# Kernel optimization log

Hardware: AMD Instinct MI355X
Metric: run time of the kernel (lower is better)

The kernel has to match this reference:

```python
import jax, jax.numpy as jnp
import numpy as np

EPS_DEMOD = 1e-8
EPS_GN = 1e-5
GROUPS = 8


def setup_inputs() -> dict:
    key = jax.random.key(0)
    ks = jax.random.split(key, 4)
    b, c, h, w = 16, 64, 256, 256
    n_kernels, c_out = 4, 64
    x = jax.random.normal(ks[0], (b, c, h, w), dtype=jnp.float32)
    mod = jax.random.normal(ks[1], (b, c), dtype=jnp.float32)
    kernel_mod = jax.random.normal(ks[2], (b, n_kernels), dtype=jnp.float32)
    # kaiming normal, fan_in = c*3*3, leaky_relu gain sqrt(2)
    std = float(np.sqrt(2.0 / (c * 9)))
    conv_weights = jax.random.normal(ks[3], (n_kernels, c_out, c, 3, 3), dtype=jnp.float32) * std
    gn_gamma = jnp.ones((c_out,), dtype=jnp.float32)
    gn_beta = jnp.zeros((c_out,), dtype=jnp.float32)
    return {"x": x, "mod": mod, "kernel_mod": kernel_mod,
            "conv_weights": conv_weights, "gn_gamma": gn_gamma, "gn_beta": gn_beta}


def _block_forward(x, mod, kernel_mod, conv_weights, gn_gamma, gn_beta):
    b = x.shape[0]
    # --- adaptive kernel selection (softmax over num_conv_kernels) ---
    kernel_attn = jax.nn.softmax(kernel_mod, axis=-1)                # [b, n]
    w = jnp.einsum('noikl,bn->boikl', conv_weights, kernel_attn)     # [b, o, i, 3, 3]
    # --- stylegan2 modulation ---
    w = w * (mod[:, None, :, None, None] + 1.0)
    # --- demodulation ---
    inv_norm = jax.lax.rsqrt(jnp.clip(jnp.sum(w * w, axis=(2, 3, 4), keepdims=True), EPS_DEMOD, None))
    w = w * inv_norm
    # --- per-sample conv (vmap over batch, SAME padding, stride 1) ---
    def conv_one(xi, wi):
        return jax.lax.conv_general_dilated(
            xi[None], wi, window_strides=(1, 1), padding='SAME',
            dimension_numbers=('NCHW', 'OIHW', 'NCHW'))[0]
    y = jax.vmap(conv_one)(x, w)                                     # [b, o, h, w]
    # --- GroupNorm(groups=8) ---
    bb, c, hh, ww = y.shape
    yg = y.reshape(bb, GROUPS, c // GROUPS, hh, ww)
    mean = jnp.mean(yg, axis=(2, 3, 4), keepdims=True)
    var = jnp.var(yg, axis=(2, 3, 4), keepdims=True)
    yg = (yg - mean) * jax.lax.rsqrt(var + EPS_GN)
    y = yg.reshape(bb, c, hh, ww) * gn_gamma[None, :, None, None] + gn_beta[None, :, None, None]
    # --- SiLU ---
    return y * jax.nn.sigmoid(y)


def reference(x, mod, kernel_mod, conv_weights, gn_gamma, gn_beta):
    return _block_forward(x, mod, kernel_mod, conv_weights, gn_gamma, gn_beta)
```

## Files before the change

kernel.cpp:

```cpp
#include <hip/hip_runtime.h>
#include <hip/hip_bf16.h>
#include <math.h>

#define B_ 16
#define C_IN 64
#define C_OUT 64
#define H_ 256
#define W_ 256
#define NK 4
#define NGROUPS 8
#define CH_PER_G (C_OUT / NGROUPS)

#define WM16_SHORTS (B_ * C_OUT * 9 * C_IN)
#define WM16_BYTES (WM16_SHORTS * 2)
#define STATS_FLOATS (B_ * NGROUPS * 2)

#define XT_PIX (258 * 258)
#define XT_OFF ((size_t)(WM16_BYTES + 4096))
#define XT_BYTES ((size_t)B_ * XT_PIX * 64 * 2)

typedef __attribute__((ext_vector_type(8))) short bf16x8;
typedef __attribute__((ext_vector_type(4))) float f32x4;
typedef unsigned int u32;

static __device__ __forceinline__ unsigned bf16bits(float v) {
    return (unsigned)__builtin_bit_cast(unsigned short, __float2bfloat16(v));
}

static __device__ __forceinline__ void load_lds16(const unsigned short* g, void* l) {
    __builtin_amdgcn_global_load_lds(
        (const __attribute__((address_space(1))) u32*)g,
        (__attribute__((address_space(3))) u32*)l, 16, 0, 0);
}

__global__ __launch_bounds__(64)
void k_weights(const float* __restrict__ mod, const float* __restrict__ kmod,
               const float* __restrict__ cw, unsigned short* __restrict__ wm16) {
    int bo = blockIdx.x;
    int b = bo >> 6, o = bo & 63;
    int lane = threadIdx.x;

    float a0 = kmod[b * NK + 0], a1 = kmod[b * NK + 1];
    float a2 = kmod[b * NK + 2], a3 = kmod[b * NK + 3];
    float m = fmaxf(fmaxf(a0, a1), fmaxf(a2, a3));
    float e0 = __expf(a0 - m), e1 = __expf(a1 - m);
    float e2 = __expf(a2 - m), e3 = __expf(a3 - m);
    float inv = 1.0f / (e0 + e1 + e2 + e3);
    e0 *= inv; e1 *= inv; e2 *= inv; e3 *= inv;

    float modv = mod[b * C_IN + lane] + 1.0f;

    float wv[9];
    float ss = 0.0f;
#pragma unroll
    for (int j = 0; j < 9; ++j) {
        int idx = o * 576 + lane * 9 + j;
        float w = cw[0 * C_OUT * 576 + idx] * e0
                + cw[1 * C_OUT * 576 + idx] * e1
                + cw[2 * C_OUT * 576 + idx] * e2
                + cw[3 * C_OUT * 576 + idx] * e3;
        w *= modv;
        wv[j] = w;
        ss += w * w;
    }
#pragma unroll
    for (int off = 32; off > 0; off >>= 1)
        ss += __shfl_xor(ss, off, 64);
    float invn = rsqrtf(fmaxf(ss, 1e-8f));
#pragma unroll
    for (int j = 0; j < 9; ++j)
        wm16[((b * 64 + o) * 9 + j) * 64 + lane] =
            (unsigned short)bf16bits(wv[j] * invn);
}

__global__ __launch_bounds__(256)
void k_border(unsigned short* __restrict__ xt) {
    int t = blockIdx.x * 256 + threadIdx.x;
    int chunk = t & 7;
    int p = t >> 3;
    int b = p / 1028;
    int pid = p - b * 1028;
    int r, c;
    if (pid < 258)      { r = 0;             c = pid; }
    else if (pid < 516) { r = 257;           c = pid - 258; }
    else if (pid < 772) { r = pid - 516 + 1; c = 0; }
    else                { r = pid - 772 + 1; c = 257; }
    *(int4*)((char*)xt + (size_t)(b * XT_PIX + r * 258 + c) * 128 + chunk * 16) =
        make_int4(0, 0, 0, 0);
}

__global__ __launch_bounds__(256)
void k_xpose(const float* __restrict__ x, unsigned short* __restrict__ xt) {
    const int bx  = blockIdx.x;
    const int seg = bx & 1;
    const int h   = (bx >> 1) & 255;
    const int b   = bx >> 9;
    const int c   = threadIdx.x & 63;
    const int wv  = threadIdx.x >> 6;
    const int p0  = seg * 128 + wv * 32;
    const float* xp = x + (((b * 64 + c) * 256 + h) * 256 + p0);
    unsigned short* op = xt + ((size_t)(b * 258 + h + 1) * 258 + p0 + 1) * 64 + c;
#pragma unroll
    for (int j = 0; j < 8; ++j) {
        float4 v = *(const float4*)(xp + j * 4);
        op[(j * 4 + 0) * 64] = (unsigned short)bf16bits(v.x);
        op[(j * 4 + 1) * 64] = (unsigned short)bf16bits(v.y);
        op[(j * 4 + 2) * 64] = (unsigned short)bf16bits(v.z);
        op[(j * 4 + 3) * 64] = (unsigned short)bf16bits(v.w);
    }
}

#define NSLOT 340
#define SLOTPAD 352

__global__ __launch_bounds__(256, 3)
void k_conv2(const unsigned short* __restrict__ xt,
             const unsigned short* __restrict__ wm16,
             float* __restrict__ y, float* __restrict__ stats) {
    __shared__ __align__(16) char smem[SLOTPAD * 128];
    __shared__ float lst[16];

    const int tile = blockIdx.x;
    const int b    = blockIdx.y;
    const int R0   = (tile >> 3) * 8;
    const int C0   = (tile & 7) * 32;
    const int tid  = threadIdx.x;
    const int w    = tid >> 6;
    const int lane = tid & 63;
    const int l15  = lane & 15;
    const int q    = lane >> 4;

    if (tid < 16) lst[tid] = 0.0f;

    const unsigned short* xb = xt + (size_t)b * (XT_PIX * 64);
#pragma unroll
    for (int k = 0; k < 11; ++k) {
        int t = k * 256 + tid;
        int slot = t >> 3;
        int p = t & 7;
        int s = slot < NSLOT ? slot : NSLOT - 1;
        int r = s / 34;
        int c = s - r * 34;
        int srcchunk = p ^ (s & 7);
        const unsigned short* src = xb + (((R0 + r) * 258 + (C0 + c)) * 64 + srcchunk * 8);
        load_lds16(src, smem + t * 16);
    }
    __syncthreads();

    f32x4 acc[4][4];
#pragma unroll
    for (int mt = 0; mt < 4; ++mt)
#pragma unroll
        for (int nt = 0; nt < 4; ++nt)
            acc[mt][nt] = (f32x4){0.f, 0.f, 0.f, 0.f};

    const unsigned short* wb = wm16 + b * (64 * 9 * 64);

    for (int tap = 0; tap < 9; ++tap) {
        const int ky = tap / 3;
        const int kx = tap - ky * 3;

        bf16x8 af[4][2];
#pragma unroll
        for (int mt = 0; mt < 4; ++mt)
#pragma unroll
            for (int kc = 0; kc < 2; ++kc)
                af[mt][kc] = *(const bf16x8*)(wb +
                    ((mt * 16 + l15) * 9 + tap) * 64 + kc * 32 + q * 8);

#pragma unroll
        for (int kc = 0; kc < 2; ++kc) {
            bf16x8 bfr[4];
#pragma unroll
            for (int nt = 0; nt < 4; ++nt) {
                int ro = 2 * w + (nt >> 1);
                int c0 = (nt & 1) * 16;
                int slot = (ro + ky) * 34 + c0 + kx + l15;
                int chunk = kc * 4 + q;
                bfr[nt] = *(const bf16x8*)(smem + slot * 128 +
                                           ((chunk ^ (slot & 7)) << 4));
            }
#pragma unroll
            for (int mt = 0; mt < 4; ++mt)
#pragma unroll
                for (int nt = 0; nt < 4; ++nt)
                    acc[mt][nt] = __builtin_amdgcn_mfma_f32_16x16x32_bf16(
                        af[mt][kc], bfr[nt], acc[mt][nt], 0, 0, 0);
        }
    }

    float sg[4] = {0.f, 0.f, 0.f, 0.f};
    float qg[4] = {0.f, 0.f, 0.f, 0.f};
#pragma unroll
    for (int mt = 0; mt < 4; ++mt) {
#pragma unroll
        for (int nt = 0; nt < 4; ++nt) {
            int ro = 2 * w + (nt >> 1);
            int c0 = (nt & 1) * 16;
            float* yp = y + ((b * 64 + mt * 16 + q * 4) * 65536 +
                             (R0 + ro) * 256 + C0 + c0 + l15);
#pragma unroll
            for (int r = 0; r < 4; ++r) {
                float v = acc[mt][nt][r];
                yp[r * 65536] = v;
                sg[mt] += v;
                qg[mt] += v * v;
            }
        }
    }
#pragma unroll
    for (int mt = 0; mt < 4; ++mt) {
#pragma unroll
        for (int off = 1; off <= 16; off <<= 1) {
            sg[mt] += __shfl_xor(sg[mt], off, 64);
            qg[mt] += __shfl_xor(qg[mt], off, 64);
        }
    }
    if ((lane & 31) == 0) {
        const int gsel = q >> 1;
#pragma unroll
        for (int mt = 0; mt < 4; ++mt) {
            atomicAdd(&lst[(2 * mt + gsel) * 2 + 0], sg[mt]);
            atomicAdd(&lst[(2 * mt + gsel) * 2 + 1], qg[mt]);
        }
    }
    __syncthreads();
    if (tid < 16) atomicAdd(&stats[b * 16 + tid], lst[tid]);
}

#define LDSBYTES (NSLOT * 128)

__global__ __launch_bounds__(256, 3)
void k_conv(const float* __restrict__ x, const unsigned short* __restrict__ wm16,
            float* __restrict__ y, float* __restrict__ stats) {
    __shared__ __align__(16) char smem[LDSBYTES];
    __shared__ float lst[16];

    const int tile = blockIdx.x;
    const int b    = blockIdx.y;
    const int R0   = (tile >> 3) * 8;
    const int C0   = (tile & 7) * 32;
    const int tid  = threadIdx.x;
    const int w    = tid >> 6;
    const int lane = tid & 63;
    const int l15  = lane & 15;
    const int q    = lane >> 4;

    if (tid < 16) lst[tid] = 0.0f;

    for (int t = tid; t < NSLOT * 8; t += 256) {
        int chunk = t / NSLOT;
        int slot  = t - chunk * NSLOT;
        int r = slot / 34;
        int c = slot - r * 34;
        int gr = R0 - 1 + r;
        int gc = C0 - 1 + c;
        bool ok = ((unsigned)gr < (unsigned)H_) && ((unsigned)gc < (unsigned)W_);
        const float* xp = x + (((b * 64 + chunk * 8) * 256 + gr) * 256 + gc);
        unsigned u[4];
#pragma unroll
        for (int jj = 0; jj < 4; ++jj) {
            float v0 = ok ? xp[(2 * jj) * 65536] : 0.0f;
            float v1 = ok ? xp[(2 * jj + 1) * 65536] : 0.0f;
            u[jj] = (bf16bits(v1) << 16) | bf16bits(v0);
        }
        *(int4*)(smem + slot * 128 + ((chunk ^ (slot & 7)) << 4)) =
            make_int4(u[0], u[1], u[2], u[3]);
    }
    __syncthreads();

    f32x4 acc[4][4];
#pragma unroll
    for (int mt = 0; mt < 4; ++mt)
#pragma unroll
        for (int nt = 0; nt < 4; ++nt)
            acc[mt][nt] = (f32x4){0.f, 0.f, 0.f, 0.f};

    const unsigned short* wb = wm16 + b * (64 * 9 * 64);

    for (int tap = 0; tap < 9; ++tap) {
        const int ky = tap / 3;
        const int kx = tap - ky * 3;

        bf16x8 af[4][2];
#pragma unroll
        for (int mt = 0; mt < 4; ++mt)
#pragma unroll
            for (int kc = 0; kc < 2; ++kc)
                af[mt][kc] = *(const bf16x8*)(wb +
                    ((mt * 16 + l15) * 9 + tap) * 64 + kc * 32 + q * 8);

#pragma unroll
        for (int kc = 0; kc < 2; ++kc) {
            bf16x8 bfr[4];
#pragma unroll
            for (int nt = 0; nt < 4; ++nt) {
                int ro = 2 * w + (nt >> 1);
                int c0 = (nt & 1) * 16;
                int slot = (ro + ky) * 34 + c0 + kx + l15;
                int chunk = kc * 4 + q;
                bfr[nt] = *(const bf16x8*)(smem + slot * 128 +
                                           ((chunk ^ (slot & 7)) << 4));
            }
#pragma unroll
            for (int mt = 0; mt < 4; ++mt)
#pragma unroll
                for (int nt = 0; nt < 4; ++nt)
                    acc[mt][nt] = __builtin_amdgcn_mfma_f32_16x16x32_bf16(
                        af[mt][kc], bfr[nt], acc[mt][nt], 0, 0, 0);
        }
    }

    float sg[4] = {0.f, 0.f, 0.f, 0.f};
    float qg[4] = {0.f, 0.f, 0.f, 0.f};
#pragma unroll
    for (int mt = 0; mt < 4; ++mt) {
#pragma unroll
        for (int nt = 0; nt < 4; ++nt) {
            int ro = 2 * w + (nt >> 1);
            int c0 = (nt & 1) * 16;
            float* yp = y + ((b * 64 + mt * 16 + q * 4) * 65536 +
                             (R0 + ro) * 256 + C0 + c0 + l15);
#pragma unroll
            for (int r = 0; r < 4; ++r) {
                float v = acc[mt][nt][r];
                yp[r * 65536] = v;
                sg[mt] += v;
                qg[mt] += v * v;
            }
        }
    }
    const int gsel = q >> 1;
#pragma unroll
    for (int mt = 0; mt < 4; ++mt) {
        atomicAdd(&lst[(2 * mt + gsel) * 2 + 0], sg[mt]);
        atomicAdd(&lst[(2 * mt + gsel) * 2 + 1], qg[mt]);
    }
    __syncthreads();
    if (tid < 16) atomicAdd(&stats[b * 16 + tid], lst[tid]);
}

__global__ __launch_bounds__(256)
void k_norm(float4* __restrict__ y, const float* __restrict__ stats,
            const float* __restrict__ gamma, const float* __restrict__ beta) {
    const int cg = blockIdx.x >> 6;
    const int b  = cg >> 6;
    const int ch = cg & 63;
    const int g  = ch >> 3;

    const float sum = stats[(b * NGROUPS + g) * 2 + 0];
    const float ssq = stats[(b * NGROUPS + g) * 2 + 1];
    const float invN = 1.0f / (float)(CH_PER_G * H_ * W_);
    const float mean = sum * invN;
    const float var  = fmaxf(ssq * invN - mean * mean, 0.0f);
    const float rstd = rsqrtf(var + 1e-5f);
    const float ga = gamma[ch] * rstd;
    const float be = beta[ch] - mean * ga;

    const int idx = blockIdx.x * 256 + threadIdx.x;
    float4 v = y[idx];
    float t;
    t = v.x * ga + be; v.x = t / (1.0f + __expf(-t));
    t = v.y * ga + be; v.y = t / (1.0f + __expf(-t));
    t = v.z * ga + be; v.z = t / (1.0f + __expf(-t));
    t = v.w * ga + be; v.w = t / (1.0f + __expf(-t));
    y[idx] = v;
}

extern "C" void kernel_launch(void* const* d_in, const int* in_sizes, int n_in,
                              void* d_out, int out_size, void* d_ws, size_t ws_size,
                              hipStream_t stream) {
    const float* x     = (const float*)d_in[0];
    const float* mod   = (const float*)d_in[1];
    const float* kmod  = (const float*)d_in[2];
    const float* cw    = (const float*)d_in[3];
    const float* gamma = (const float*)d_in[4];
    const float* beta  = (const float*)d_in[5];
    float* out = (float*)d_out;

    unsigned short* wm16 = (unsigned short*)d_ws;
    float* stats = (float*)((char*)d_ws + WM16_BYTES);
    unsigned short* xt = (unsigned short*)((char*)d_ws + XT_OFF);

    k_weights<<<dim3(B_ * C_OUT), dim3(64), 0, stream>>>(mod, kmod, cw, wm16);
    hipMemsetAsync(stats, 0, STATS_FLOATS * sizeof(float), stream);

    if (ws_size >= XT_OFF + XT_BYTES) {
        k_border<<<dim3(514), dim3(256), 0, stream>>>(xt);
        k_xpose<<<dim3(8192), dim3(256), 0, stream>>>(x, xt);
        k_conv2<<<dim3(256, B_), dim3(256), 0, stream>>>(xt, wm16, out, stats);
    } else {
        k_conv<<<dim3(256, B_), dim3(256), 0, stream>>>(x, wm16, out, stats);
    }

    k_norm<<<dim3(B_ * C_OUT * 64), dim3(256), 0, stream>>>(
        (float4*)out, stats, gamma, beta);
}
```

Measured before the change: 746.9 us.

## Split conv input staging into two channel halves, swap MFMA operands, fuse launches

New measurement: 1.597 ms. 2.14x slower.

```diff
diff --git a/kernel.cpp b/kernel.cpp
--- a/kernel.cpp
+++ b/kernel.cpp
@@ -35,8 +35,10 @@
 
 __global__ __launch_bounds__(64)
 void k_weights(const float* __restrict__ mod, const float* __restrict__ kmod,
-               const float* __restrict__ cw, unsigned short* __restrict__ wm16) {
+               const float* __restrict__ cw, unsigned short* __restrict__ wm16,
+               float* __restrict__ stats) {
     int bo = blockIdx.x;
+    if (bo < 4) stats[bo * 64 + threadIdx.x] = 0.0f;
     int b = bo >> 6, o = bo & 63;
     int lane = threadIdx.x;
 
@@ -74,24 +76,23 @@
 }
 
 __global__ __launch_bounds__(256)
-void k_border(unsigned short* __restrict__ xt) {
-    int t = blockIdx.x * 256 + threadIdx.x;
-    int chunk = t & 7;
-    int p = t >> 3;
-    int b = p / 1028;
-    int pid = p - b * 1028;
-    int r, c;
-    if (pid < 258)      { r = 0;             c = pid; }
-    else if (pid < 516) { r = 257;           c = pid - 258; }
-    else if (pid < 772) { r = pid - 516 + 1; c = 0; }
-    else                { r = pid - 772 + 1; c = 257; }
-    *(int4*)((char*)xt + (size_t)(b * XT_PIX + r * 258 + c) * 128 + chunk * 16) =
-        make_int4(0, 0, 0, 0);
-}
-
-__global__ __launch_bounds__(256)
 void k_xpose(const float* __restrict__ x, unsigned short* __restrict__ xt) {
-    const int bx  = blockIdx.x;
+    const int bx = blockIdx.x;
+    if (bx >= 8192) {
+        int t = (bx - 8192) * 256 + threadIdx.x;
+        int chunk = t & 7;
+        int p = t >> 3;
+        int b = p / 1028;
+        int pid = p - b * 1028;
+        int r, c;
+        if (pid < 258)      { r = 0;             c = pid; }
+        else if (pid < 516) { r = 257;           c = pid - 258; }
+        else if (pid < 772) { r = pid - 516 + 1; c = 0; }
+        else                { r = pid - 772 + 1; c = 257; }
+        *(int4*)((char*)xt + (size_t)(b * XT_PIX + r * 258 + c) * 128 + chunk * 16) =
+            make_int4(0, 0, 0, 0);
+        return;
+    }
     const int seg = bx & 1;
     const int h   = (bx >> 1) & 255;
     const int b   = bx >> 9;
@@ -111,13 +112,13 @@
 }
 
 #define NSLOT 340
-#define SLOTPAD 352
-
-__global__ __launch_bounds__(256, 3)
+#define STAGE_T 1536
+
+__global__ __launch_bounds__(256, 6)
 void k_conv2(const unsigned short* __restrict__ xt,
              const unsigned short* __restrict__ wm16,
              float* __restrict__ y, float* __restrict__ stats) {
-    __shared__ __align__(16) char smem[SLOTPAD * 128];
+    __shared__ __align__(16) char smem[STAGE_T * 16];
     __shared__ float lst[16];
 
     const int tile = blockIdx.x;
@@ -133,19 +134,7 @@
     if (tid < 16) lst[tid] = 0.0f;
 
     const unsigned short* xb = xt + (size_t)b * (XT_PIX * 64);
-#pragma unroll
-    for (int k = 0; k < 11; ++k) {
-        int t = k * 256 + tid;
-        int slot = t >> 3;
-        int p = t & 7;
-        int s = slot < NSLOT ? slot : NSLOT - 1;
-        int r = s / 34;
-        int c = s - r * 34;
-        int srcchunk = p ^ (s & 7);
-        const unsigned short* src = xb + (((R0 + r) * 258 + (C0 + c)) * 64 + srcchunk * 8);
-        load_lds16(src, smem + t * 16);
-    }
-    __syncthreads();
+    const unsigned short* wb = wm16 + b * (64 * 9 * 64);
 
     f32x4 acc[4][4];
 #pragma unroll
@@ -154,38 +143,48 @@
         for (int nt = 0; nt < 4; ++nt)
             acc[mt][nt] = (f32x4){0.f, 0.f, 0.f, 0.f};
 
-    const unsigned short* wb = wm16 + b * (64 * 9 * 64);
-
-    for (int tap = 0; tap < 9; ++tap) {
-        const int ky = tap / 3;
-        const int kx = tap - ky * 3;
-
-        bf16x8 af[4][2];
-#pragma unroll
-        for (int mt = 0; mt < 4; ++mt)
-#pragma unroll
-            for (int kc = 0; kc < 2; ++kc)
-                af[mt][kc] = *(const bf16x8*)(wb +
-                    ((mt * 16 + l15) * 9 + tap) * 64 + kc * 32 + q * 8);
-
-#pragma unroll
-        for (int kc = 0; kc < 2; ++kc) {
-            bf16x8 bfr[4];
+    for (int h = 0; h < 2; ++h) {
+        if (h) __syncthreads();
+
+#pragma unroll
+        for (int k = 0; k < 6; ++k) {
+            int t = k * 256 + tid;
+            int slot = t >> 2;
+            int p = t & 3;
+            int s = slot < NSLOT ? slot : NSLOT - 1;
+            int r = s / 34;
+            int c = s - r * 34;
+            const unsigned short* src = xb +
+                (((R0 + r) * 258 + (C0 + c)) * 64 + h * 32 + ((p ^ (s & 3)) << 3));
+            load_lds16(src, smem + t * 16);
+        }
+        __syncthreads();
+
+        for (int tap = 0; tap < 9; ++tap) {
+            const int ky = tap / 3;
+            const int kx = tap - ky * 3;
+
+            bf16x8 wf[4];
+#pragma unroll
+            for (int mt = 0; mt < 4; ++mt)
+                wf[mt] = *(const bf16x8*)(wb +
+                    ((mt * 16 + l15) * 9 + tap) * 64 + h * 32 + q * 8);
+
+            bf16x8 ax[4];
 #pragma unroll
             for (int nt = 0; nt < 4; ++nt) {
                 int ro = 2 * w + (nt >> 1);
                 int c0 = (nt & 1) * 16;
                 int slot = (ro + ky) * 34 + c0 + kx + l15;
-                int chunk = kc * 4 + q;
-                bfr[nt] = *(const bf16x8*)(smem + slot * 128 +
-                                           ((chunk ^ (slot & 7)) << 4));
+                ax[nt] = *(const bf16x8*)(smem + slot * 64 +
+                                          ((q ^ (slot & 3)) << 4));
             }
 #pragma unroll
             for (int mt = 0; mt < 4; ++mt)
 #pragma unroll
                 for (int nt = 0; nt < 4; ++nt)
                     acc[mt][nt] = __builtin_amdgcn_mfma_f32_16x16x32_bf16(
-                        af[mt][kc], bfr[nt], acc[mt][nt], 0, 0, 0);
+                        ax[nt], wf[mt], acc[mt][nt], 0, 0, 0);
         }
     }
 
@@ -197,27 +196,24 @@
         for (int nt = 0; nt < 4; ++nt) {
             int ro = 2 * w + (nt >> 1);
             int c0 = (nt & 1) * 16;
-            float* yp = y + ((b * 64 + mt * 16 + q * 4) * 65536 +
-                             (R0 + ro) * 256 + C0 + c0 + l15);
-#pragma unroll
-            for (int r = 0; r < 4; ++r) {
-                float v = acc[mt][nt][r];
-                yp[r * 65536] = v;
-                sg[mt] += v;
-                qg[mt] += v * v;
-            }
+            float* yp = y + ((b * 64 + mt * 16 + l15) * 65536 +
+                             (R0 + ro) * 256 + C0 + c0 + q * 4);
+            f32x4 v = acc[mt][nt];
+            *(f32x4*)yp = v;
+            sg[mt] += v[0] + v[1] + v[2] + v[3];
+            qg[mt] += v[0]*v[0] + v[1]*v[1] + v[2]*v[2] + v[3]*v[3];
         }
     }
 #pragma unroll
     for (int mt = 0; mt < 4; ++mt) {
-#pragma unroll
-        for (int off = 1; off <= 16; off <<= 1) {
-            sg[mt] += __shfl_xor(sg[mt], off, 64);
-            qg[mt] += __shfl_xor(qg[mt], off, 64);
-        }
-    }
-    if ((lane & 31) == 0) {
-        const int gsel = q >> 1;
+        sg[mt] += __shfl_xor(sg[mt], 1, 64);  qg[mt] += __shfl_xor(qg[mt], 1, 64);
+        sg[mt] += __shfl_xor(sg[mt], 2, 64);  qg[mt] += __shfl_xor(qg[mt], 2, 64);
+        sg[mt] += __shfl_xor(sg[mt], 4, 64);  qg[mt] += __shfl_xor(qg[mt], 4, 64);
+        sg[mt] += __shfl_xor(sg[mt], 16, 64); qg[mt] += __shfl_xor(qg[mt], 16, 64);
+        sg[mt] += __shfl_xor(sg[mt], 32, 64); qg[mt] += __shfl_xor(qg[mt], 32, 64);
+    }
+    if ((lane & 55) == 0) {
+        const int gsel = (lane >> 3) & 1;
 #pragma unroll
         for (int mt = 0; mt < 4; ++mt) {
             atomicAdd(&lst[(2 * mt + gsel) * 2 + 0], sg[mt]);
@@ -343,7 +339,7 @@
 __global__ __launch_bounds__(256)
 void k_norm(float4* __restrict__ y, const float* __restrict__ stats,
             const float* __restrict__ gamma, const float* __restrict__ beta) {
-    const int cg = blockIdx.x >> 6;
+    const int cg = blockIdx.x;
     const int b  = cg >> 6;
     const int ch = cg & 63;
     const int g  = ch >> 3;
@@ -357,14 +353,17 @@
     const float ga = gamma[ch] * rstd;
     const float be = beta[ch] - mean * ga;
 
-    const int idx = blockIdx.x * 256 + threadIdx.x;
-    float4 v = y[idx];
-    float t;
-    t = v.x * ga + be; v.x = t / (1.0f + __expf(-t));
-    t = v.y * ga + be; v.y = t / (1.0f + __expf(-t));
-    t = v.z * ga + be; v.z = t / (1.0f + __expf(-t));
-    t = v.w * ga + be; v.w = t / (1.0f + __expf(-t));
-    y[idx] = v;
+    float4* p = y + (size_t)cg * 16384;
+#pragma unroll 4
+    for (int i = threadIdx.x; i < 16384; i += 256) {
+        float4 v = p[i];
+        float t;
+        t = v.x * ga + be; v.x = t / (1.0f + __expf(-t));
+        t = v.y * ga + be; v.y = t / (1.0f + __expf(-t));
+        t = v.z * ga + be; v.z = t / (1.0f + __expf(-t));
+        t = v.w * ga + be; v.w = t / (1.0f + __expf(-t));
+        p[i] = v;
+    }
 }
 
 extern "C" void kernel_launch(void* const* d_in, const int* in_sizes, int n_in,
@@ -382,17 +381,15 @@
     float* stats = (float*)((char*)d_ws + WM16_BYTES);
     unsigned short* xt = (unsigned short*)((char*)d_ws + XT_OFF);
 
-    k_weights<<<dim3(B_ * C_OUT), dim3(64), 0, stream>>>(mod, kmod, cw, wm16);
-    hipMemsetAsync(stats, 0, STATS_FLOATS * sizeof(float), stream);
+    k_weights<<<dim3(B_ * C_OUT), dim3(64), 0, stream>>>(mod, kmod, cw, wm16, stats);
 
     if (ws_size >= XT_OFF + XT_BYTES) {
-        k_border<<<dim3(514), dim3(256), 0, stream>>>(xt);
-        k_xpose<<<dim3(8192), dim3(256), 0, stream>>>(x, xt);
+        k_xpose<<<dim3(8192 + 514), dim3(256), 0, stream>>>(x, xt);
         k_conv2<<<dim3(256, B_), dim3(256), 0, stream>>>(xt, wm16, out, stats);
     } else {
         k_conv<<<dim3(256, B_), dim3(256), 0, stream>>>(x, wm16, out, stats);
     }
 
-    k_norm<<<dim3(B_ * C_OUT * 64), dim3(256), 0, stream>>>(
+    k_norm<<<dim3(B_ * C_OUT), dim3(256), 0, stream>>>(
         (float4*)out, stats, gamma, beta);
 }
```
